# Kernel optimization log

Measured on AMD Instinct MI355X. Metric: run time of the kernel, lower is better.

Reference implementation:

```python
import jax, jax.numpy as jnp
import numpy as np

HIDDEN = 2048
NUM_HEADS = 32
HEAD_DIM = 64
NUM_KV = 8
GROUP = NUM_HEADS // NUM_KV
SCALE = HEAD_DIM ** -0.5
ROPE_BASE = 10000.0


def apply_rope(t):
    # t: [B, H, S, D]; standard half-split rotary embedding
    S, D = t.shape[-2], t.shape[-1]
    inv_freq = 1.0 / (ROPE_BASE ** (jnp.arange(0, D, 2, dtype=jnp.float32) / D))  # [D/2]
    ang = jnp.arange(S, dtype=jnp.float32)[:, None] * inv_freq[None, :]           # [S, D/2]
    cos, sin = jnp.cos(ang), jnp.sin(ang)
    x1, x2 = t[..., : D // 2], t[..., D // 2 :]
    return jnp.concatenate([x1 * cos - x2 * sin, x2 * cos + x1 * sin], axis=-1)


def setup_inputs() -> dict:
    key = jax.random.key(0)
    ks = jax.random.split(key, 10)
    B, S = 2, 2048
    s_in = HIDDEN ** -0.5
    s_o = (NUM_HEADS * HEAD_DIM) ** -0.5
    return {
        "x": jax.random.normal(ks[0], (B, S, HIDDEN), jnp.float32),
        "Wq": jax.random.normal(ks[1], (NUM_HEADS * HEAD_DIM, HIDDEN), jnp.float32) * s_in,
        "bq": jnp.zeros((NUM_HEADS * HEAD_DIM,), jnp.float32),
        "Wk": jax.random.normal(ks[2], (NUM_KV * HEAD_DIM, HIDDEN), jnp.float32) * s_in,
        "bk": jnp.zeros((NUM_KV * HEAD_DIM,), jnp.float32),
        "Wv": jax.random.normal(ks[3], (NUM_KV * HEAD_DIM, HIDDEN), jnp.float32) * s_in,
        "bv": jnp.zeros((NUM_KV * HEAD_DIM,), jnp.float32),
        "Wo": jax.random.normal(ks[4], (HIDDEN, NUM_HEADS * HEAD_DIM), jnp.float32) * s_o,
        "bo": jnp.zeros((HIDDEN,), jnp.float32),
        "key_weights": jax.random.normal(ks[5], (NUM_HEADS,), jnp.float32),
    }


def reference(x, Wq, bq, Wk, bk, Wv, bv, Wo, bo, key_weights):
    B, S, _ = x.shape
    q = (x @ Wq.T + bq).reshape(B, S, NUM_HEADS, HEAD_DIM).transpose(0, 2, 1, 3)
    k = (x @ Wk.T + bk).reshape(B, S, NUM_KV, HEAD_DIM).transpose(0, 2, 1, 3)
    v = (x @ Wv.T + bv).reshape(B, S, NUM_KV, HEAD_DIM).transpose(0, 2, 1, 3)
    q = apply_rope(q)
    k = apply_rope(k)
    # group queries per KV head: [B, kv, g, S, D]
    qg = q.reshape(B, NUM_KV, GROUP, S, HEAD_DIM)
    scores = jnp.einsum("bkgsd,bktd->bkgst", qg, k) * SCALE
    scores = scores * key_weights.reshape(1, NUM_KV, GROUP, 1, 1)
    causal = jnp.tril(jnp.ones((S, S), bool))
    scores = jnp.where(causal, scores, -jnp.inf)
    a = jax.nn.softmax(scores, axis=-1)
    o = jnp.einsum("bkgst,bktd->bkgsd", a, v)  # [B, kv, g, S, D]
    o = o.reshape(B, NUM_HEADS, S, HEAD_DIM).transpose(0, 2, 1, 3).reshape(B, S, NUM_HEADS * HEAD_DIM)
    return o @ Wo.T + bo
```

## Files before the change

### kernel.cpp

```cpp
#include <hip/hip_runtime.h>
#include <stdint.h>

#define S_LEN 2048
#define HID   2048
#define NH    32
#define NKV   8
#define HD    64
#define BATCH 2
#define NROWS (BATCH * S_LEN)
#define QKVN  (NH*HD + 2*NKV*HD)

typedef unsigned short u16;
typedef __bf16 bf16_t;
typedef bf16_t bf16x8 __attribute__((ext_vector_type(8)));
typedef float  f32x4  __attribute__((ext_vector_type(4)));
typedef float  f32x16 __attribute__((ext_vector_type(16)));
typedef u16    u16x8  __attribute__((ext_vector_type(8)));

#define LOG2E 1.4426950408889634f

__device__ __forceinline__ u16 f2bf(float f) {
    union { float f; uint32_t u; } v; v.f = f;
    uint32_t u = v.u;
    return (u16)((u + 0x7fffu + ((u >> 16) & 1u)) >> 16);
}

__device__ __forceinline__ unsigned cvtpk(float a, float b) {
    unsigned r;
    asm("v_cvt_pk_bf16_f32 %0, %1, %2" : "=v"(r) : "v"(a), "v"(b));
    return r;
}

__device__ __forceinline__ void plswap(unsigned &a, unsigned &b) {
    asm volatile("v_permlane32_swap_b32 %0, %1" : "+v"(a), "+v"(b));
}

__device__ __forceinline__ void llds16(const void* g, void* l) {
    __builtin_amdgcn_global_load_lds(
        (const __attribute__((address_space(1))) void*)g,
        (__attribute__((address_space(3))) void*)l,
        16, 0, 0);
}

#define CBAR(N) do { \
    asm volatile("s_waitcnt vmcnt(" #N ")" ::: "memory"); \
    __builtin_amdgcn_s_barrier(); \
    __builtin_amdgcn_sched_barrier(0); \
} while (0)

__global__ void cvt_all(const float* __restrict__ x, const float* __restrict__ wq,
                        const float* __restrict__ wk, const float* __restrict__ wv,
                        const float* __restrict__ wo,
                        u16* __restrict__ xb, u16* __restrict__ wqkvb, u16* __restrict__ wob) {
    int e = blockIdx.x * 256 + threadIdx.x;
    const float* s; u16* d; int o;
    if (e < 1048576)      { s = x;  d = xb;                 o = e; }
    else if (e < 1572864) { s = wq; d = wqkvb;              o = e - 1048576; }
    else if (e < 1703936) { s = wk; d = wqkvb + 2048*2048;  o = e - 1572864; }
    else if (e < 1835008) { s = wv; d = wqkvb + 2560*2048;  o = e - 1703936; }
    else                  { s = wo; d = wob;                o = e - 1835008; }
    const float4* sp = (const float4*)s;
    float4 a = sp[2*(size_t)o], b = sp[2*(size_t)o + 1];
    u16x8 r;
    r[0]=f2bf(a.x); r[1]=f2bf(a.y); r[2]=f2bf(a.z); r[3]=f2bf(a.w);
    r[4]=f2bf(b.x); r[5]=f2bf(b.y); r[6]=f2bf(b.z); r[7]=f2bf(b.w);
    *(u16x8*)(d + 8*(size_t)o) = r;
}

__global__ void build_bqkv(const float* __restrict__ bq, const float* __restrict__ bk,
                           const float* __restrict__ bv, float* __restrict__ bqkv) {
    int i = blockIdx.x * 256 + threadIdx.x;
    if (i >= QKVN) return;
    bqkv[i] = (i < 2048) ? bq[i] : (i < 2560 ? bk[i - 2048] : bv[i - 2560]);
}

__global__ void rope_table(float* __restrict__ tab) {
    int idx = blockIdx.x * 256 + threadIdx.x;
    if (idx >= S_LEN * 32) return;
    int i = idx & 31, s = idx >> 5;
    float invf = exp2f(-(float)i * (13.287712379549449f / 32.0f));
    float ang = (float)s * invf;
    float sn, cs;
    sincosf(ang, &sn, &cs);
    tab[idx] = cs;
    tab[S_LEN*32 + idx] = sn;
}

__global__ __launch_bounds__(256) void gemm_qkv(
    const u16* __restrict__ A, const u16* __restrict__ Bw,
    const float* __restrict__ bias, const float* __restrict__ rtab,
    const float* __restrict__ kw,
    u16* __restrict__ qpk, u16* __restrict__ kpk, u16* __restrict__ vlin)
{
    const int M = NROWS, N = QKVN, K = HID;
    const int nbm = M >> 7, nbn = N >> 7;
    const int nwg = nbm * nbn;
    int wg = blockIdx.x;
    wg = (wg & 7) * (nwg >> 3) + (wg >> 3);
    const int bm = wg % nbm, bn = wg / nbm;
    const int brow = bm << 7, bcol = bn << 7;

    __shared__ u16 sbuf[3][8192];

    const int t = threadIdx.x;
    const int lane = t & 63, wid = t >> 6;
    const int wr = wid >> 1, wc = wid & 1;
    const int lr = lane & 15, lhi = lane >> 4;

    auto stage = [&](int kt, int bi) {
        const int k0 = kt << 5;
        #pragma unroll
        for (int i = 0; i < 2; ++i) {
            const unsigned off = ((unsigned)t << 4) + ((unsigned)i << 12);
            const unsigned row = off >> 6;
            const unsigned ce  = (off & 63) >> 1;
            llds16(A  + (size_t)(brow + row) * K + (k0 + ce), &sbuf[bi][0]    + (off >> 1));
            llds16(Bw + (size_t)(bcol + row) * K + (k0 + ce), &sbuf[bi][4096] + (off >> 1));
        }
    };

    f32x4 acc[4][4] = {};
    const int nk = K >> 5;

    stage(0, 0);
    stage(1, 1);
    int cur = 0, st2 = 2;
    for (int kt = 0; kt < nk; ++kt) {
        if (kt < nk - 1) CBAR(4); else CBAR(0);
        if (kt + 2 < nk) stage(kt + 2, st2);
        const u16* sA = &sbuf[cur][0];
        const u16* sB = &sbuf[cur][4096];
        bf16x8 af[4], bfv[4];
        #pragma unroll
        for (int m = 0; m < 4; ++m)
            af[m] = *(const bf16x8*)(sA + ((wr*64 + m*16 + lr) * 32 + lhi*8));
        #pragma unroll
        for (int n = 0; n < 4; ++n)
            bfv[n] = *(const bf16x8*)(sB + ((wc*64 + n*16 + lr) * 32 + lhi*8));
        #pragma unroll
        for (int m = 0; m < 4; ++m)
            #pragma unroll
            for (int n = 0; n < 4; ++n)
                acc[m][n] = __builtin_amdgcn_mfma_f32_16x16x32_bf16(af[m], bfv[n], acc[m][n], 0, 0, 0);
        cur = (cur == 2) ? 0 : cur + 1;
        st2 = (st2 == 2) ? 0 : st2 + 1;
    }

    const int c64 = bcol + wc*64;
    const int hb  = c64 >> 6;
    const int rowb = brow + wr*64;

    if (hb < 40) {
        const bool isQ = hb < 32;
        const float sc = isQ ? (0.125f * LOG2E * kw[hb]) : 1.0f;
        u16* dst = isQ ? qpk : kpk;
        const int nheads = isQ ? 32 : 8;
        const int hloc = isQ ? hb : (hb - 32);
        #pragma unroll
        for (int m = 0; m < 4; ++m) {
            #pragma unroll
            for (int n = 0; n < 2; ++n) {
                const int i = n*16 + lr;
                const float b1 = bias[c64 + i];
                const float b2 = bias[c64 + i + 32];
                #pragma unroll
                for (int j = 0; j < 4; ++j) {
                    const int row = rowb + m*16 + lhi*4 + j;
                    const int s = row & (S_LEN - 1);
                    const int bb = row >> 11;
                    const float x1 = acc[m][n][j] + b1;
                    const float x2 = acc[m][n+2][j] + b2;
                    const float cs = rtab[s*32 + i];
                    const float sn = rtab[S_LEN*32 + s*32 + i];
                    const size_t base = ((size_t)(bb*nheads + hloc)) * (S_LEN*64) + (size_t)s*64;
                    dst[base + i]      = f2bf((x1*cs - x2*sn) * sc);
                    dst[base + i + 32] = f2bf((x2*cs + x1*sn) * sc);
                }
            }
        }
    } else {
        #pragma unroll
        for (int m = 0; m < 4; ++m) {
            #pragma unroll
            for (int n = 0; n < 4; ++n) {
                const int col = c64 + n*16 + lr;
                const float bv = bias[col];
                #pragma unroll
                for (int j = 0; j < 4; ++j) {
                    const int row = rowb + m*16 + lhi*4 + j;
                    vlin[(size_t)row * 512 + (col - 2560)] = f2bf(acc[m][n][j] + bv);
                }
            }
        }
    }
}

__global__ __launch_bounds__(256) void gemm_bt(
    const u16* __restrict__ A, const u16* __restrict__ Bw,
    const float* __restrict__ bias, float* __restrict__ C,
    int M, int N, int K)
{
    const int nbm = M >> 7, nbn = N >> 7;
    const int nwg = nbm * nbn;
    int wg = blockIdx.x;
    wg = (wg & 7) * (nwg >> 3) + (wg >> 3);
    const int bm = wg % nbm, bn = wg / nbm;
    const int brow = bm << 7, bcol = bn << 7;

    __shared__ u16 sbuf[3][8192];

    const int t = threadIdx.x;
    const int lane = t & 63, wid = t >> 6;
    const int wr = wid >> 1, wc = wid & 1;
    const int lr = lane & 15, lhi = lane >> 4;

    auto stage = [&](int kt, int bi) {
        const int k0 = kt << 5;
        #pragma unroll
        for (int i = 0; i < 2; ++i) {
            const unsigned off = ((unsigned)t << 4) + ((unsigned)i << 12);
            const unsigned row = off >> 6;
            const unsigned ce  = (off & 63) >> 1;
            llds16(A  + (size_t)(brow + row) * K + (k0 + ce), &sbuf[bi][0]    + (off >> 1));
            llds16(Bw + (size_t)(bcol + row) * K + (k0 + ce), &sbuf[bi][4096] + (off >> 1));
        }
    };

    f32x4 acc[4][4] = {};
    const int nk = K >> 5;

    stage(0, 0);
    stage(1, 1);
    int cur = 0, st2 = 2;
    for (int kt = 0; kt < nk; ++kt) {
        if (kt < nk - 1) CBAR(4); else CBAR(0);
        if (kt + 2 < nk) stage(kt + 2, st2);
        const u16* sA = &sbuf[cur][0];
        const u16* sB = &sbuf[cur][4096];
        bf16x8 af[4], bfv[4];
        #pragma unroll
        for (int m = 0; m < 4; ++m)
            af[m] = *(const bf16x8*)(sA + ((wr*64 + m*16 + lr) * 32 + lhi*8));
        #pragma unroll
        for (int n = 0; n < 4; ++n)
            bfv[n] = *(const bf16x8*)(sB + ((wc*64 + n*16 + lr) * 32 + lhi*8));
        #pragma unroll
        for (int m = 0; m < 4; ++m)
            #pragma unroll
            for (int n = 0; n < 4; ++n)
                acc[m][n] = __builtin_amdgcn_mfma_f32_16x16x32_bf16(af[m], bfv[n], acc[m][n], 0, 0, 0);
        cur = (cur == 2) ? 0 : cur + 1;
        st2 = (st2 == 2) ? 0 : st2 + 1;
    }

    #pragma unroll
    for (int m = 0; m < 4; ++m) {
        #pragma unroll
        for (int n = 0; n < 4; ++n) {
            const int col = bcol + wc*64 + n*16 + lr;
            const float bv = bias[col];
            #pragma unroll
            for (int j = 0; j < 4; ++j) {
                const int row = brow + wr*64 + m*16 + lhi*4 + j;
                C[(size_t)row * N + col] = acc[m][n][j] + bv;
            }
        }
    }
}

__global__ void pack_vt(const u16* __restrict__ vlin, u16* __restrict__ vtb) {
    __shared__ u16 tile[64][67];
    const int st = blockIdx.x;
    const int bk = blockIdx.y;
    const int t = threadIdx.x;
    const int b = bk >> 3, kvh = bk & 7;
    const int r = t >> 2, cg = (t & 3) << 4;
    const u16* src = vlin + ((size_t)(b*S_LEN + st*64 + r)) * 512 + kvh*64 + cg;
    #pragma unroll
    for (int j = 0; j < 16; ++j) tile[r][cg + j] = src[j];
    __syncthreads();
    const int d = t >> 2, sg = (t & 3) << 4;
    u16* dst = vtb + ((size_t)(bk*64 + d)) * S_LEN + st*64 + sg;
    #pragma unroll
    for (int j = 0; j < 16; ++j) dst[j] = tile[sg + j][d];
}

__global__ __launch_bounds__(512, 4) void attn_fwd(
    const u16* __restrict__ Q,
    const u16* __restrict__ Kk,
    const u16* __restrict__ Vt,
    u16* __restrict__ O)
{
    __shared__ u16 sK[3][64 * 64];
    __shared__ u16 sV[3][64 * 64];

    const int t = threadIdx.x;
    const int lane = t & 63, wid = t >> 6;
    const int hi = lane >> 5, lq = lane & 31;
    const int bid = blockIdx.x;
    const int qb = (bid < 256) ? (7 - (bid >> 6)) : ((bid >> 6) - 4);
    const int bh = bid & 63;
    const int b = bh >> 5, h = bh & 31;
    const int kvh = h >> 2;

    const u16* Kp = Kk + ((size_t)(b*NKV + kvh)) * (S_LEN * 64);
    const u16* Vp = Vt + ((size_t)(b*NKV + kvh)) * (64 * S_LEN);

    const int q0w = qb*256 + wid*32;
    const int qg  = q0w + lq;

    const u16* Qrow = Q + (((size_t)bh) * S_LEN + qg) * 64 + 8*hi;
    bf16x8 qf[4];
    #pragma unroll
    for (int kd = 0; kd < 4; ++kd)
        qf[kd] = *(const bf16x8*)(Qrow + 16*kd);

    f32x16 accO0 = {}, accO1 = {};
    float m_run = 0.f, l_run = 0.f;

    const int ntB = 4*qb + 4;
    const int tmax_w = (q0w + 31) >> 6;

    auto stageKV = [&](int kt, int bi) {
        const int kv = kt << 6;
        const unsigned row = t >> 3, cb = (t & 7) << 4;
        const unsigned scb = cb ^ ((row & 7) << 4);
        llds16(Kp + (size_t)(kv + row) * 64 + (scb >> 1), &sK[bi][0] + t*8);
        llds16(Vp + (size_t)row * S_LEN + kv + (scb >> 1), &sV[bi][0] + t*8);
    };

    stageKV(0, 0);
    stageKV(1, 1);
    int cur = 0, st2 = 2;

    for (int tt = 0; tt < ntB; ++tt) {
        if (tt < ntB - 1) CBAR(2); else CBAR(0);
        if (tt + 2 < ntB) stageKV(tt + 2, st2);
        if (tt <= tmax_w) {
            const int kv0 = tt * 64;
            const float nm = -m_run;
            f32x16 s0, s1;
            #pragma unroll
            for (int r = 0; r < 16; ++r) { s0[r] = nm; s1[r] = nm; }
            #pragma unroll
            for (int kd = 0; kd < 4; ++kd) {
                const unsigned bc = ((unsigned)(32*kd + 16*hi)) ^ ((lq & 7) << 4);
                bf16x8 k0 = *(const bf16x8*)((const char*)&sK[cur][0] + lq*128 + bc);
                bf16x8 k1 = *(const bf16x8*)((const char*)&sK[cur][0] + (32 + lq)*128 + bc);
                s0 = __builtin_amdgcn_mfma_f32_32x32x16_bf16(k0, qf[kd], s0, 0, 0, 0);
                s1 = __builtin_amdgcn_mfma_f32_32x32x16_bf16(k1, qf[kd], s1, 0, 0, 0);
            }
            if (kv0 + 63 > q0w) {
                #pragma unroll
                for (int r = 0; r < 16; ++r) {
                    const int kvg = kv0 + (r & 3) + 8*(r >> 2) + 4*hi;
                    if (kvg > qg)      s0[r] = -INFINITY;
                    if (kvg + 32 > qg) s1[r] = -INFINITY;
                }
            }
            float mx[8];
            #pragma unroll
            for (int r = 0; r < 8; ++r)
                mx[r] = fmaxf(fmaxf(s0[r], s0[r+8]), fmaxf(s1[r], s1[r+8]));
            float tm = fmaxf(fmaxf(fmaxf(mx[0], mx[1]), fmaxf(mx[2], mx[3])),
                             fmaxf(fmaxf(mx[4], mx[5]), fmaxf(mx[6], mx[7])));
            tm = fmaxf(tm, __shfl_xor(tm, 32));
            if (!__all(tm <= 8.0f)) {
                const float dd = fmaxf(tm, 0.f);
                const float al = __builtin_amdgcn_exp2f(-dd);
                m_run += dd;
                l_run *= al;
                #pragma unroll
                for (int r = 0; r < 16; ++r) { accO0[r] *= al; accO1[r] *= al; }
                #pragma unroll
                for (int r = 0; r < 16; ++r) { s0[r] -= dd; s1[r] -= dd; }
            }
            #pragma unroll
            for (int r = 0; r < 16; ++r) {
                s0[r] = __builtin_amdgcn_exp2f(s0[r]);
                s1[r] = __builtin_amdgcn_exp2f(s1[r]);
            }
            float sm[8];
            #pragma unroll
            for (int r = 0; r < 8; ++r)
                sm[r] = (s0[r] + s0[r+8]) + (s1[r] + s1[r+8]);
            float rs = ((sm[0]+sm[1]) + (sm[2]+sm[3])) + ((sm[4]+sm[5]) + (sm[6]+sm[7]));
            rs += __shfl_xor(rs, 32);
            l_run += rs;

            #pragma unroll
            for (int ks = 0; ks < 4; ++ks) {
                const f32x16& e = (ks & 2) ? s1 : s0;
                const int rb = (ks & 1) * 8;
                unsigned x0 = cvtpk(e[rb + 0], e[rb + 1]);
                unsigned x1 = cvtpk(e[rb + 2], e[rb + 3]);
                unsigned y0 = cvtpk(e[rb + 4], e[rb + 5]);
                unsigned y1 = cvtpk(e[rb + 6], e[rb + 7]);
                plswap(x0, y0);
                plswap(x1, y1);
                union { unsigned u[4]; bf16x8 v; } pb;
                pb.u[0] = x0; pb.u[1] = x1; pb.u[2] = y0; pb.u[3] = y1;
                const unsigned bc = ((unsigned)(32*ks + 16*hi)) ^ ((lq & 7) << 4);
                bf16x8 v0 = *(const bf16x8*)((const char*)&sV[cur][0] + lq*128 + bc);
                bf16x8 v1 = *(const bf16x8*)((const char*)&sV[cur][0] + (32 + lq)*128 + bc);
                accO0 = __builtin_amdgcn_mfma_f32_32x32x16_bf16(v0, pb.v, accO0, 0, 0, 0);
                accO1 = __builtin_amdgcn_mfma_f32_32x32x16_bf16(v1, pb.v, accO1, 0, 0, 0);
            }
        }
        cur = (cur == 2) ? 0 : cur + 1;
        st2 = (st2 == 2) ? 0 : st2 + 1;
    }

    const float inv = 1.0f / l_run;
    u16* orow = O + (((size_t)(b * S_LEN) + q0w + lq)) * (NH*HD) + h*64;
    #pragma unroll
    for (int g = 0; g < 4; ++g) {
        uint2 w0, w1;
        w0.x = cvtpk(accO0[4*g + 0] * inv, accO0[4*g + 1] * inv);
        w0.y = cvtpk(accO0[4*g + 2] * inv, accO0[4*g + 3] * inv);
        *(uint2*)(orow + 8*g + 4*hi) = w0;
        w1.x = cvtpk(accO1[4*g + 0] * inv, accO1[4*g + 1] * inv);
        w1.y = cvtpk(accO1[4*g + 2] * inv, accO1[4*g + 3] * inv);
        *(uint2*)(orow + 32 + 8*g + 4*hi) = w1;
    }
}

extern "C" void kernel_launch(void* const* d_in, const int* in_sizes, int n_in,
                              void* d_out, int out_size, void* d_ws, size_t ws_size,
                              hipStream_t stream) {
    const float* x  = (const float*)d_in[0];
    const float* Wq = (const float*)d_in[1];
    const float* bq = (const float*)d_in[2];
    const float* Wk = (const float*)d_in[3];
    const float* bk = (const float*)d_in[4];
    const float* Wv = (const float*)d_in[5];
    const float* bv = (const float*)d_in[6];
    const float* Wo = (const float*)d_in[7];
    const float* bo = (const float*)d_in[8];
    const float* kw = (const float*)d_in[9];

    uint8_t* ws = (uint8_t*)d_ws;
    u16*   xb    = (u16*)(ws);
    u16*   wqkvb = (u16*)(ws + 16777216);
    u16*   wob   = (u16*)(ws + 29360128);
    u16*   qpk   = (u16*)(ws + 37748736);
    u16*   kpk   = (u16*)(ws + 54525952);
    u16*   vlin  = (u16*)(ws + 58720256);
    u16*   vtb   = (u16*)(ws + 62914560);
    u16*   ob    = (u16*)(ws + 67108864);
    float* bqkv  = (float*)(ws + 83886080);
    float* rtab  = (float*)(ws + 83898368);

    cvt_all<<<9216, 256, 0, stream>>>(x, Wq, Wk, Wv, Wo, xb, wqkvb, wob);
    build_bqkv<<<12, 256, 0, stream>>>(bq, bk, bv, bqkv);
    rope_table<<<256, 256, 0, stream>>>(rtab);

    gemm_qkv<<<768, 256, 0, stream>>>(xb, wqkvb, bqkv, rtab, kw, qpk, kpk, vlin);

    pack_vt<<<dim3(32, 16), 256, 0, stream>>>(vlin, vtb);

    attn_fwd<<<dim3(512), dim3(512), 0, stream>>>(qpk, kpk, vtb, ob);

    gemm_bt<<<512, 256, 0, stream>>>(ob, wob, bo, (float*)d_out, NROWS, HID, HID);

    (void)in_sizes; (void)n_in; (void)out_size; (void)ws_size;
}
```

Before: 194.1 us.

## Widen GEMM tiles to 128x256, swizzle LDS layout, and merge prep kernels

Both bf16 GEMMs now use 128x256 output tiles, with each wave computing 64x128 and an XOR-swizzled LDS layout intended to reduce bank conflicts on fragment reads. Grids drop from 768/512 to 384/256 workgroups, and launch_bounds now requests 2 waves per SIMD. The three prep kernels (convert, bias build, rope table) are fused into one launch to cut launch overhead. The larger tiles raise register and LDS pressure and halve the number of workgroups, which could underfill 256 CUs.

```diff
diff --git a/kernel.cpp b/kernel.cpp
--- a/kernel.cpp
+++ b/kernel.cpp
@@ -48,63 +48,63 @@
     __builtin_amdgcn_sched_barrier(0); \
 } while (0)
 
-__global__ void cvt_all(const float* __restrict__ x, const float* __restrict__ wq,
-                        const float* __restrict__ wk, const float* __restrict__ wv,
-                        const float* __restrict__ wo,
-                        u16* __restrict__ xb, u16* __restrict__ wqkvb, u16* __restrict__ wob) {
+#define CVT_GROUPS 2359296
+__global__ void prep_all(const float* __restrict__ x, const float* __restrict__ wq,
+                         const float* __restrict__ wk, const float* __restrict__ wv,
+                         const float* __restrict__ wo,
+                         const float* __restrict__ bq, const float* __restrict__ bk,
+                         const float* __restrict__ bv,
+                         u16* __restrict__ xb, u16* __restrict__ wqkvb, u16* __restrict__ wob,
+                         float* __restrict__ rtab, float* __restrict__ bqkv) {
     int e = blockIdx.x * 256 + threadIdx.x;
-    const float* s; u16* d; int o;
-    if (e < 1048576)      { s = x;  d = xb;                 o = e; }
-    else if (e < 1572864) { s = wq; d = wqkvb;              o = e - 1048576; }
-    else if (e < 1703936) { s = wk; d = wqkvb + 2048*2048;  o = e - 1572864; }
-    else if (e < 1835008) { s = wv; d = wqkvb + 2560*2048;  o = e - 1703936; }
-    else                  { s = wo; d = wob;                o = e - 1835008; }
-    const float4* sp = (const float4*)s;
-    float4 a = sp[2*(size_t)o], b = sp[2*(size_t)o + 1];
-    u16x8 r;
-    r[0]=f2bf(a.x); r[1]=f2bf(a.y); r[2]=f2bf(a.z); r[3]=f2bf(a.w);
-    r[4]=f2bf(b.x); r[5]=f2bf(b.y); r[6]=f2bf(b.z); r[7]=f2bf(b.w);
-    *(u16x8*)(d + 8*(size_t)o) = r;
-}
-
-__global__ void build_bqkv(const float* __restrict__ bq, const float* __restrict__ bk,
-                           const float* __restrict__ bv, float* __restrict__ bqkv) {
-    int i = blockIdx.x * 256 + threadIdx.x;
-    if (i >= QKVN) return;
-    bqkv[i] = (i < 2048) ? bq[i] : (i < 2560 ? bk[i - 2048] : bv[i - 2560]);
-}
-
-__global__ void rope_table(float* __restrict__ tab) {
-    int idx = blockIdx.x * 256 + threadIdx.x;
-    if (idx >= S_LEN * 32) return;
-    int i = idx & 31, s = idx >> 5;
-    float invf = exp2f(-(float)i * (13.287712379549449f / 32.0f));
-    float ang = (float)s * invf;
-    float sn, cs;
-    sincosf(ang, &sn, &cs);
-    tab[idx] = cs;
-    tab[S_LEN*32 + idx] = sn;
-}
-
-__global__ __launch_bounds__(256) void gemm_qkv(
+    if (e < CVT_GROUPS) {
+        const float* s; u16* d; int o;
+        if (e < 1048576)      { s = x;  d = xb;                 o = e; }
+        else if (e < 1572864) { s = wq; d = wqkvb;              o = e - 1048576; }
+        else if (e < 1703936) { s = wk; d = wqkvb + 2048*2048;  o = e - 1572864; }
+        else if (e < 1835008) { s = wv; d = wqkvb + 2560*2048;  o = e - 1703936; }
+        else                  { s = wo; d = wob;                o = e - 1835008; }
+        const float4* sp = (const float4*)s;
+        float4 a = sp[2*(size_t)o], b = sp[2*(size_t)o + 1];
+        u16x8 r;
+        r[0]=f2bf(a.x); r[1]=f2bf(a.y); r[2]=f2bf(a.z); r[3]=f2bf(a.w);
+        r[4]=f2bf(b.x); r[5]=f2bf(b.y); r[6]=f2bf(b.z); r[7]=f2bf(b.w);
+        *(u16x8*)(d + 8*(size_t)o) = r;
+    } else if (e < CVT_GROUPS + 65536) {
+        int idx = e - CVT_GROUPS;
+        int i = idx & 31, s = idx >> 5;
+        float invf = exp2f(-(float)i * (13.287712379549449f / 32.0f));
+        float ang = (float)s * invf;
+        float sn, cs;
+        sincosf(ang, &sn, &cs);
+        rtab[idx] = cs;
+        rtab[S_LEN*32 + idx] = sn;
+    } else if (e < CVT_GROUPS + 65536 + QKVN) {
+        int i = e - CVT_GROUPS - 65536;
+        bqkv[i] = (i < 2048) ? bq[i] : (i < 2560 ? bk[i - 2048] : bv[i - 2560]);
+    }
+}
+
+
+__global__ __launch_bounds__(256, 2) void gemm_qkv(
     const u16* __restrict__ A, const u16* __restrict__ Bw,
     const float* __restrict__ bias, const float* __restrict__ rtab,
     const float* __restrict__ kw,
     u16* __restrict__ qpk, u16* __restrict__ kpk, u16* __restrict__ vlin)
 {
     const int M = NROWS, N = QKVN, K = HID;
-    const int nbm = M >> 7, nbn = N >> 7;
+    const int nbm = M >> 7, nbn = N >> 8;
     const int nwg = nbm * nbn;
     int wg = blockIdx.x;
     wg = (wg & 7) * (nwg >> 3) + (wg >> 3);
     const int bm = wg % nbm, bn = wg / nbm;
-    const int brow = bm << 7, bcol = bn << 7;
-
-    __shared__ u16 sbuf[3][8192];
+    const int brow = bm << 7, bcol = bn << 8;
+
+    __shared__ u16 sbuf[3][12288];
 
     const int t = threadIdx.x;
     const int lane = t & 63, wid = t >> 6;
-    const int wr = wid >> 1, wc = wid & 1;
+    const int wr = wid >> 1, wn = wid & 1;
     const int lr = lane & 15, lhi = lane >> 4;
 
     auto stage = [&](int kt, int bi) {
@@ -113,105 +113,118 @@
         for (int i = 0; i < 2; ++i) {
             const unsigned off = ((unsigned)t << 4) + ((unsigned)i << 12);
             const unsigned row = off >> 6;
-            const unsigned ce  = (off & 63) >> 1;
-            llds16(A  + (size_t)(brow + row) * K + (k0 + ce), &sbuf[bi][0]    + (off >> 1));
-            llds16(Bw + (size_t)(bcol + row) * K + (k0 + ce), &sbuf[bi][4096] + (off >> 1));
+            const unsigned scb = (off & 63) ^ ((row & 3) << 4);
+            llds16(A + (size_t)(brow + row) * K + (k0 + (scb >> 1)), &sbuf[bi][0] + (off >> 1));
+        }
+        #pragma unroll
+        for (int i = 0; i < 4; ++i) {
+            const unsigned off = ((unsigned)t << 4) + ((unsigned)i << 12);
+            const unsigned row = off >> 6;
+            const unsigned scb = (off & 63) ^ ((row & 3) << 4);
+            llds16(Bw + (size_t)(bcol + row) * K + (k0 + (scb >> 1)), &sbuf[bi][4096] + (off >> 1));
         }
     };
 
-    f32x4 acc[4][4] = {};
+    f32x4 acc[4][8] = {};
     const int nk = K >> 5;
 
     stage(0, 0);
     stage(1, 1);
     int cur = 0, st2 = 2;
     for (int kt = 0; kt < nk; ++kt) {
-        if (kt < nk - 1) CBAR(4); else CBAR(0);
+        if (kt < nk - 1) CBAR(6); else CBAR(0);
         if (kt + 2 < nk) stage(kt + 2, st2);
-        const u16* sA = &sbuf[cur][0];
-        const u16* sB = &sbuf[cur][4096];
-        bf16x8 af[4], bfv[4];
+        const char* sA = (const char*)&sbuf[cur][0];
+        const char* sB = (const char*)&sbuf[cur][4096];
+        bf16x8 af[4], bfv[8];
+        #pragma unroll
+        for (int m = 0; m < 4; ++m) {
+            const int row = wr*64 + m*16 + lr;
+            af[m] = *(const bf16x8*)(sA + row*64 + ((lhi*16) ^ ((row & 3) << 4)));
+        }
+        #pragma unroll
+        for (int n = 0; n < 8; ++n) {
+            const int row = wn*128 + n*16 + lr;
+            bfv[n] = *(const bf16x8*)(sB + row*64 + ((lhi*16) ^ ((row & 3) << 4)));
+        }
         #pragma unroll
         for (int m = 0; m < 4; ++m)
-            af[m] = *(const bf16x8*)(sA + ((wr*64 + m*16 + lr) * 32 + lhi*8));
-        #pragma unroll
-        for (int n = 0; n < 4; ++n)
-            bfv[n] = *(const bf16x8*)(sB + ((wc*64 + n*16 + lr) * 32 + lhi*8));
-        #pragma unroll
-        for (int m = 0; m < 4; ++m)
-            #pragma unroll
-            for (int n = 0; n < 4; ++n)
+            #pragma unroll
+            for (int n = 0; n < 8; ++n)
                 acc[m][n] = __builtin_amdgcn_mfma_f32_16x16x32_bf16(af[m], bfv[n], acc[m][n], 0, 0, 0);
         cur = (cur == 2) ? 0 : cur + 1;
         st2 = (st2 == 2) ? 0 : st2 + 1;
     }
 
-    const int c64 = bcol + wc*64;
-    const int hb  = c64 >> 6;
     const int rowb = brow + wr*64;
-
-    if (hb < 40) {
-        const bool isQ = hb < 32;
-        const float sc = isQ ? (0.125f * LOG2E * kw[hb]) : 1.0f;
-        u16* dst = isQ ? qpk : kpk;
-        const int nheads = isQ ? 32 : 8;
-        const int hloc = isQ ? hb : (hb - 32);
-        #pragma unroll
-        for (int m = 0; m < 4; ++m) {
-            #pragma unroll
-            for (int n = 0; n < 2; ++n) {
-                const int i = n*16 + lr;
-                const float b1 = bias[c64 + i];
-                const float b2 = bias[c64 + i + 32];
+    #pragma unroll
+    for (int hg = 0; hg < 2; ++hg) {
+        const int c64 = bcol + wn*128 + hg*64;
+        const int hb  = c64 >> 6;
+        if (hb < 40) {
+            const bool isQ = hb < 32;
+            const float sc = isQ ? (0.125f * LOG2E * kw[hb]) : 1.0f;
+            u16* dst = isQ ? qpk : kpk;
+            const int nheads = isQ ? 32 : 8;
+            const int hloc = isQ ? hb : (hb - 32);
+            #pragma unroll
+            for (int m = 0; m < 4; ++m) {
                 #pragma unroll
-                for (int j = 0; j < 4; ++j) {
-                    const int row = rowb + m*16 + lhi*4 + j;
-                    const int s = row & (S_LEN - 1);
-                    const int bb = row >> 11;
-                    const float x1 = acc[m][n][j] + b1;
-                    const float x2 = acc[m][n+2][j] + b2;
-                    const float cs = rtab[s*32 + i];
-                    const float sn = rtab[S_LEN*32 + s*32 + i];
-                    const size_t base = ((size_t)(bb*nheads + hloc)) * (S_LEN*64) + (size_t)s*64;
-                    dst[base + i]      = f2bf((x1*cs - x2*sn) * sc);
-                    dst[base + i + 32] = f2bf((x2*cs + x1*sn) * sc);
+                for (int nn = 0; nn < 2; ++nn) {
+                    const int n = 4*hg + nn;
+                    const int i = nn*16 + lr;
+                    const float b1 = bias[c64 + i];
+                    const float b2 = bias[c64 + i + 32];
+                    #pragma unroll
+                    for (int j = 0; j < 4; ++j) {
+                        const int row = rowb + m*16 + lhi*4 + j;
+                        const int s = row & (S_LEN - 1);
+                        const int bb = row >> 11;
+                        const float x1 = acc[m][n][j] + b1;
+                        const float x2 = acc[m][n+2][j] + b2;
+                        const float cs = rtab[s*32 + i];
+                        const float sn = rtab[S_LEN*32 + s*32 + i];
+                        const size_t base = ((size_t)(bb*nheads + hloc)) * (S_LEN*64) + (size_t)s*64;
+                        dst[base + i]      = f2bf((x1*cs - x2*sn) * sc);
+                        dst[base + i + 32] = f2bf((x2*cs + x1*sn) * sc);
+                    }
                 }
             }
-        }
-    } else {
-        #pragma unroll
-        for (int m = 0; m < 4; ++m) {
-            #pragma unroll
-            for (int n = 0; n < 4; ++n) {
-                const int col = c64 + n*16 + lr;
-                const float bv = bias[col];
+        } else {
+            #pragma unroll
+            for (int m = 0; m < 4; ++m) {
                 #pragma unroll
-                for (int j = 0; j < 4; ++j) {
-                    const int row = rowb + m*16 + lhi*4 + j;
-                    vlin[(size_t)row * 512 + (col - 2560)] = f2bf(acc[m][n][j] + bv);
+                for (int nn = 0; nn < 4; ++nn) {
+                    const int col = c64 + nn*16 + lr;
+                    const float bv = bias[col];
+                    #pragma unroll
+                    for (int j = 0; j < 4; ++j) {
+                        const int row = rowb + m*16 + lhi*4 + j;
+                        vlin[(size_t)row * 512 + (col - 2560)] = f2bf(acc[m][nn + 4*hg][j] + bv);
+                    }
                 }
             }
         }
     }
 }
 
-__global__ __launch_bounds__(256) void gemm_bt(
+__global__ __launch_bounds__(256, 2) void gemm_bt(
     const u16* __restrict__ A, const u16* __restrict__ Bw,
     const float* __restrict__ bias, float* __restrict__ C,
     int M, int N, int K)
 {
-    const int nbm = M >> 7, nbn = N >> 7;
+    const int nbm = M >> 7, nbn = N >> 8;
     const int nwg = nbm * nbn;
     int wg = blockIdx.x;
     wg = (wg & 7) * (nwg >> 3) + (wg >> 3);
     const int bm = wg % nbm, bn = wg / nbm;
-    const int brow = bm << 7, bcol = bn << 7;
-
-    __shared__ u16 sbuf[3][8192];
+    const int brow = bm << 7, bcol = bn << 8;
+
+    __shared__ u16 sbuf[3][12288];
 
     const int t = threadIdx.x;
     const int lane = t & 63, wid = t >> 6;
-    const int wr = wid >> 1, wc = wid & 1;
+    const int wr = wid >> 1, wn = wid & 1;
     const int lr = lane & 15, lhi = lane >> 4;
 
     auto stage = [&](int kt, int bi) {
@@ -220,34 +233,44 @@
         for (int i = 0; i < 2; ++i) {
             const unsigned off = ((unsigned)t << 4) + ((unsigned)i << 12);
             const unsigned row = off >> 6;
-            const unsigned ce  = (off & 63) >> 1;
-            llds16(A  + (size_t)(brow + row) * K + (k0 + ce), &sbuf[bi][0]    + (off >> 1));
-            llds16(Bw + (size_t)(bcol + row) * K + (k0 + ce), &sbuf[bi][4096] + (off >> 1));
+            const unsigned scb = (off & 63) ^ ((row & 3) << 4);
+            llds16(A + (size_t)(brow + row) * K + (k0 + (scb >> 1)), &sbuf[bi][0] + (off >> 1));
+        }
+        #pragma unroll
+        for (int i = 0; i < 4; ++i) {
+            const unsigned off = ((unsigned)t << 4) + ((unsigned)i << 12);
+            const unsigned row = off >> 6;
+            const unsigned scb = (off & 63) ^ ((row & 3) << 4);
+            llds16(Bw + (size_t)(bcol + row) * K + (k0 + (scb >> 1)), &sbuf[bi][4096] + (off >> 1));
         }
     };
 
-    f32x4 acc[4][4] = {};
+    f32x4 acc[4][8] = {};
     const int nk = K >> 5;
 
     stage(0, 0);
     stage(1, 1);
     int cur = 0, st2 = 2;
     for (int kt = 0; kt < nk; ++kt) {
-        if (kt < nk - 1) CBAR(4); else CBAR(0);
+        if (kt < nk - 1) CBAR(6); else CBAR(0);
         if (kt + 2 < nk) stage(kt + 2, st2);
-        const u16* sA = &sbuf[cur][0];
-        const u16* sB = &sbuf[cur][4096];
-        bf16x8 af[4], bfv[4];
+        const char* sA = (const char*)&sbuf[cur][0];
+        const char* sB = (const char*)&sbuf[cur][4096];
+        bf16x8 af[4], bfv[8];
+        #pragma unroll
+        for (int m = 0; m < 4; ++m) {
+            const int row = wr*64 + m*16 + lr;
+            af[m] = *(const bf16x8*)(sA + row*64 + ((lhi*16) ^ ((row & 3) << 4)));
+        }
+        #pragma unroll
+        for (int n = 0; n < 8; ++n) {
+            const int row = wn*128 + n*16 + lr;
+            bfv[n] = *(const bf16x8*)(sB + row*64 + ((lhi*16) ^ ((row & 3) << 4)));
+        }
         #pragma unroll
         for (int m = 0; m < 4; ++m)
-            af[m] = *(const bf16x8*)(sA + ((wr*64 + m*16 + lr) * 32 + lhi*8));
-        #pragma unroll
-        for (int n = 0; n < 4; ++n)
-            bfv[n] = *(const bf16x8*)(sB + ((wc*64 + n*16 + lr) * 32 + lhi*8));
-        #pragma unroll
-        for (int m = 0; m < 4; ++m)
-            #pragma unroll
-            for (int n = 0; n < 4; ++n)
+            #pragma unroll
+            for (int n = 0; n < 8; ++n)
                 acc[m][n] = __builtin_amdgcn_mfma_f32_16x16x32_bf16(af[m], bfv[n], acc[m][n], 0, 0, 0);
         cur = (cur == 2) ? 0 : cur + 1;
         st2 = (st2 == 2) ? 0 : st2 + 1;
@@ -256,8 +279,8 @@
     #pragma unroll
     for (int m = 0; m < 4; ++m) {
         #pragma unroll
-        for (int n = 0; n < 4; ++n) {
-            const int col = bcol + wc*64 + n*16 + lr;
+        for (int n = 0; n < 8; ++n) {
+            const int col = bcol + wn*128 + n*16 + lr;
             const float bv = bias[col];
             #pragma unroll
             for (int j = 0; j < 4; ++j) {
@@ -451,17 +474,16 @@
     float* bqkv  = (float*)(ws + 83886080);
     float* rtab  = (float*)(ws + 83898368);
 
-    cvt_all<<<9216, 256, 0, stream>>>(x, Wq, Wk, Wv, Wo, xb, wqkvb, wob);
-    build_bqkv<<<12, 256, 0, stream>>>(bq, bk, bv, bqkv);
-    rope_table<<<256, 256, 0, stream>>>(rtab);
-
-    gemm_qkv<<<768, 256, 0, stream>>>(xb, wqkvb, bqkv, rtab, kw, qpk, kpk, vlin);
+    prep_all<<<9484, 256, 0, stream>>>(x, Wq, Wk, Wv, Wo, bq, bk, bv,
+                                       xb, wqkvb, wob, rtab, bqkv);
+
+    gemm_qkv<<<384, 256, 0, stream>>>(xb, wqkvb, bqkv, rtab, kw, qpk, kpk, vlin);
 
     pack_vt<<<dim3(32, 16), 256, 0, stream>>>(vlin, vtb);
 
     attn_fwd<<<dim3(512), dim3(512), 0, stream>>>(qpk, kpk, vtb, ob);
 
-    gemm_bt<<<512, 256, 0, stream>>>(ob, wob, bo, (float*)d_out, NROWS, HID, HID);
+    gemm_bt<<<256, 256, 0, stream>>>(ob, wob, bo, (float*)d_out, NROWS, HID, HID);
 
     (void)in_sizes; (void)n_in; (void)out_size; (void)ws_size;
 }
```

After: 191.5 us. Within noise of the previous version (-1.3%).
